# Optimization experiments

Measured on AMD Instinct MI355X. Metric: run time of the kernel, lower is better.

## Reference

```python
import jax, jax.numpy as jnp
import numpy as np

B, T, I, H, O = 64, 256, 128, 512, 64
GRAD_CLIP = 5.0


def setup_inputs() -> dict:
    key = jax.random.key(0)
    ks = jax.random.split(key, 20)
    sH = 1.0 / np.sqrt(H)
    sI = 1.0 / np.sqrt(I)
    f32 = jnp.float32
    return {
        "x": jax.random.normal(ks[0], (B, T, I), f32),
        "y": jax.random.randint(ks[1], (B,), 0, O),
        "W1w": jax.random.normal(ks[2], (H, H), f32) * sH,
        "V1w": jax.random.normal(ks[3], (H, I), f32) * sI,
        "V1b": jnp.zeros((H,), f32),
        "W2w": jax.random.normal(ks[4], (H, H), f32) * sH,
        "W2b": jnp.zeros((H,), f32),
        "V2w": jax.random.normal(ks[5], (H, I), f32) * sI,
        "W3w": jax.random.normal(ks[6], (H, H), f32) * sH,
        "W3b": jnp.zeros((H,), f32),
        "V3w": jax.random.normal(ks[7], (H, I), f32) * sI,
        "Woutw": jax.random.normal(ks[8], (O, H), f32) * sH,
        "Woutb": jnp.zeros((O,), f32),
        "BW1": jax.random.normal(ks[9], (O, H), f32) * sH,
        "BV1": jax.random.normal(ks[10], (O, H), f32) * sH,
        "BW2": jax.random.normal(ks[11], (O, H), f32) * sH,
        "BV2": jax.random.normal(ks[12], (O, H), f32) * sH,
        "BW3": jax.random.normal(ks[13], (O, H), f32) * sH,
        "BV3": jax.random.normal(ks[14], (O, H), f32) * sH,
    }


def reference(x, y, W1w, V1w, V1b, W2w, W2b, V2w, W3w, W3b, V3w,
              Woutw, Woutb, BW1, BV1, BW2, BV2, BW3, BV3):
    Bsz, Tlen, _ = x.shape
    Hd = W1w.shape[0]
    Od = Woutw.shape[0]
    h0 = jnp.zeros((Bsz, Hd), x.dtype)
    xt = jnp.swapaxes(x, 0, 1)  # [T, B, I]

    def step(h, xti):
        z = jax.nn.sigmoid(h @ W2w.T + W2b + xti @ V2w.T)
        r = jax.nn.sigmoid(h @ W3w.T + W3b + xti @ V3w.T)
        ht = jnp.tanh(xti @ V1w.T + V1b + (h * r) @ W1w.T)
        hn = (1.0 - z) * ht + z * h
        return hn, (r, z, ht, hn)

    hT, (rs, zs, hs, hid) = jax.lax.scan(step, h0, xt)  # each [T, B, H]
    output = jax.nn.softmax(hT @ Woutw.T + Woutb, axis=-1)
    error = output - jax.nn.one_hot(y, Od, dtype=output.dtype)

    BW1e, BV1e = error @ BW1, error @ BV1
    BW2e, BV2e = error @ BW2, error @ BV2
    BW3e, BV3e = error @ BW3, error @ BV3

    hiddens = jnp.concatenate([h0[None], hid], axis=0)  # [T+1, B, H]
    # Faithfully replicate torch's hiddens[t-1] list indexing: at t=0 this is
    # hiddens[-1], i.e. the FINAL hidden state (Python negative indexing).
    idx = (np.arange(Tlen) - 1) % (Tlen + 1)
    hprev = hiddens[idx]  # [T, B, H]

    rr = rs * (1.0 - rs)
    sz = 1.0 - zs
    dh = 1.0 - hs ** 2

    # z-gate terms (index 1) -- original code uses r*(1-r) here, replicated.
    zg = (hprev - hs) * rr
    zgV = zg * BV2e[None]
    zgW = zg * BW2e[None]
    dV1 = jnp.einsum('tbh,tbi->hi', zgV, xt) / Bsz
    dW1 = jnp.einsum('tbh,tbH->hH', zgW, hprev) / Bsz
    db1 = zgV.sum(0).mean(0)

    # r-gate terms (index 2)
    AV = ((BV3e[None] * sz * dh) @ W1w.T) * hprev * rr
    AW = ((BW3e[None] * sz * dh) @ W1w.T) * hprev * rr
    dV2 = jnp.einsum('tbh,tbi->hi', AV, xt) / Bsz
    dW2 = jnp.einsum('tbh,tbH->hH', AW, hprev) / Bsz
    db2 = AV.sum(0).mean(0)

    # h-gate terms (index 0)
    HV = ((BV1e[None] * sz) @ W1w.T) * dh
    HW = ((BW1e[None] * sz) @ W1w.T) * dh
    dV0 = jnp.einsum('tbh,tbi->hi', HV, xt) / Bsz
    dW0 = jnp.einsum('tbh,tbH->hH', HW, rs * hprev) / Bsz
    db0 = HV.sum(0).mean(0)

    def nc(g):
        g = g / jnp.linalg.norm(g)
        return jnp.clip(g, -GRAD_CLIP, GRAD_CLIP)

    return (output, hT,
            nc(dW0), nc(dW1), nc(dW2),
            nc(dV0), nc(dV1), nc(dV2),
            nc(db0), nc(db1), nc(db2),
            error)
```

## Files before the change

### kernel.cpp

```cpp
#include <hip/hip_runtime.h>
#include <hip/hip_bf16.h>

#define DI __device__ __forceinline__

typedef __bf16 bf16x8 __attribute__((ext_vector_type(8)));
typedef __bf16 bf16x4 __attribute__((ext_vector_type(4)));
typedef __bf16 bf16x2 __attribute__((ext_vector_type(2)));
typedef float  f32x4  __attribute__((ext_vector_type(4)));
typedef unsigned long long ull;

static constexpr int Bc = 64, Tc = 256, Ic = 128, Hc = 512, Oc = 64;
static constexpr int TBc = Tc * Bc;
static constexpr size_t THW = (size_t)TBc * Hc;

static constexpr size_t O_OUT = 0;
static constexpr size_t O_HT  = 4096;
static constexpr size_t O_DW0 = 36864;
static constexpr size_t O_DV0 = 823296;
static constexpr size_t O_DB0 = 1019904;
static constexpr size_t O_ERR = 1021440;

static constexpr size_t W_CTR  = 0;
static constexpr size_t W_SLOT = 1024;
static constexpr size_t W_DB   = 2048;
static constexpr size_t W_FLG  = 8192;
static constexpr size_t W_ERRW = 16384;
static constexpr size_t W_PROJ = 32768;
static constexpr size_t W_W1B  = 819200;
static constexpr size_t W_HX   = 1343488;
static constexpr size_t W_HRX  = 1474560;
static constexpr size_t W_XT   = 1605632;
static constexpr size_t W_HIST = 5799936;
static constexpr size_t W_PB   = 72908800;
static constexpr size_t W_NEED = W_PB + 100663296;


DI void st32_agent(float* p, float v) {
  __hip_atomic_store((unsigned int*)p, __float_as_uint(v),
                     __ATOMIC_RELAXED, __HIP_MEMORY_SCOPE_AGENT);
}
DI ull ld64_agent(const void* p) {
  return __hip_atomic_load((ull*)p, __ATOMIC_RELAXED, __HIP_MEMORY_SCOPE_AGENT);
}

DI void group_barrier(int* flags_g, int myslot, int bar, bool& dead) {
  __syncthreads();
  if (threadIdx.x == 0)
    __hip_atomic_store(&flags_g[myslot * 32], bar,
                       __ATOMIC_RELAXED, __HIP_MEMORY_SCOPE_AGENT);
  if (threadIdx.x < 64 && !dead) {
    const int l = threadIdx.x;
    int spins = 0;
    for (;;) {
      int v = bar;
      if (l < 16)
        v = __hip_atomic_load(&flags_g[l * 32],
                              __ATOMIC_RELAXED, __HIP_MEMORY_SCOPE_AGENT);
      if (__all(v >= bar)) break;
      __builtin_amdgcn_s_sleep(1);
      if (++spins > 4000000) { dead = true; break; }
    }
  }
  __syncthreads();
}

DI float hprev_at(const __bf16* __restrict__ h_h, int k, int col) {
  int t = k >> 6;
  if (t == 1) return 0.f;
  int row = (t == 0) ? (16320 + (k & 63)) : (k - 128);
  return (float)h_h[(size_t)row * 512 + col];
}


__global__ void kzero(float* __restrict__ p, int n) {
  int i = blockIdx.x * 256 + threadIdx.x;
  if (i < n) p[i] = 0.f;
}
__global__ void ksent(float* p, float v) { p[0] = v; }
__global__ void k0_cast(const float* __restrict__ s, __bf16* __restrict__ d, int n) {
  int i = blockIdx.x * 256 + threadIdx.x;
  if (i < n) d[i] = (__bf16)s[i];
}

__global__ __launch_bounds__(256)
void k1_xv(const float* __restrict__ x, const float* __restrict__ V1w,
           const float* __restrict__ V2w, const float* __restrict__ V3w,
           const float* __restrict__ V1b, const float* __restrict__ W2b,
           const float* __restrict__ W3b,
           float* __restrict__ xv1f, float* __restrict__ xv2f, float* __restrict__ xv3f)
{
  const int cb = blockIdx.x, t = blockIdx.y;
  const int g = cb >> 3, jblk = cb & 7;
  const float* Vg   = (g == 0) ? V1w : (g == 1) ? V2w : V3w;
  const float* bias = (g == 0) ? V1b : (g == 1) ? W2b : W3b;
  float* of = (g == 0) ? xv1f : (g == 1) ? xv2f : xv3f;
  __shared__ float As[64 * 69];
  __shared__ float Bs[64 * 69];
  const int tid = threadIdx.x;
  float acc[4][4] = {};
  const int m0 = (tid & 15) * 4, j0 = (tid >> 4) * 4;
  for (int kc = 0; kc < 2; ++kc) {
    __syncthreads();
    #pragma unroll
    for (int e = 0; e < 4; ++e) {
      int idx = tid + e * 256;
      int row = idx >> 4, c4 = (idx & 15) * 4;
      float4 v = *reinterpret_cast<const float4*>(&x[((size_t)row * 256 + t) * 128 + kc * 64 + c4]);
      As[row * 69 + c4 + 0] = v.x; As[row * 69 + c4 + 1] = v.y;
      As[row * 69 + c4 + 2] = v.z; As[row * 69 + c4 + 3] = v.w;
      float4 w = *reinterpret_cast<const float4*>(&Vg[(size_t)(jblk * 64 + row) * 128 + kc * 64 + c4]);
      Bs[row * 69 + c4 + 0] = w.x; Bs[row * 69 + c4 + 1] = w.y;
      Bs[row * 69 + c4 + 2] = w.z; Bs[row * 69 + c4 + 3] = w.w;
    }
    __syncthreads();
    for (int i = 0; i < 64; ++i) {
      float a[4], b[4];
      #pragma unroll
      for (int u = 0; u < 4; ++u) a[u] = As[(m0 + u) * 69 + i];
      #pragma unroll
      for (int u = 0; u < 4; ++u) b[u] = Bs[(j0 + u) * 69 + i];
      #pragma unroll
      for (int mi = 0; mi < 4; ++mi)
        #pragma unroll
        for (int ji = 0; ji < 4; ++ji) acc[mi][ji] += a[mi] * b[ji];
    }
  }
  #pragma unroll
  for (int ji = 0; ji < 4; ++ji) {
    int jg = jblk * 64 + j0 + ji;
    float bv = bias[jg];
    #pragma unroll
    for (int mi = 0; mi < 4; ++mi) {
      int b = m0 + mi;
      of[((size_t)t * 64 + b) * 512 + jg] = acc[mi][ji] + bv;
    }
  }
}

__global__ void e0_xt(const float* __restrict__ x, __bf16* __restrict__ XT)
{
  const int t = blockIdx.x;
  __shared__ __bf16 xs[64 * 132];
  const int tid = threadIdx.x;
  #pragma unroll
  for (int e = 0; e < 8; ++e) {
    int idx = tid + e * 256;
    int b = idx >> 5, c4 = (idx & 31) * 4;
    float4 v = *reinterpret_cast<const float4*>(&x[((size_t)b * 256 + t) * 128 + c4]);
    xs[b * 132 + c4 + 0] = (__bf16)v.x; xs[b * 132 + c4 + 1] = (__bf16)v.y;
    xs[b * 132 + c4 + 2] = (__bf16)v.z; xs[b * 132 + c4 + 3] = (__bf16)v.w;
  }
  __syncthreads();
  #pragma unroll
  for (int e = 0; e < 8; ++e) {
    int idx = tid + e * 256;
    int i = idx >> 4, b4 = (idx & 15) * 4;
    __bf16* d = &XT[(size_t)i * TBc + t * 64 + b4];
    d[0] = xs[(b4 + 0) * 132 + i];
    d[1] = xs[(b4 + 1) * 132 + i];
    d[2] = xs[(b4 + 2) * 132 + i];
    d[3] = xs[(b4 + 3) * 132 + i];
  }
}

__global__ __launch_bounds__(256, 1)
void k2_recur(const float* __restrict__ W1w, const float* __restrict__ W2w,
              const float* __restrict__ W3w,
              const float* __restrict__ xv1, const float* __restrict__ xv2,
              const float* __restrict__ xv3,
              __bf16* __restrict__ r_h, __bf16* __restrict__ z_h,
              __bf16* __restrict__ ht_h, __bf16* __restrict__ h_h,
              float* __restrict__ hx, float* __restrict__ hrx,
              int* __restrict__ flags, float* __restrict__ dout)
{
  const int g  = blockIdx.x >> 4;
  const int cw = blockIdx.x & 15;
  const int tid = threadIdx.x, lane = tid & 63, wv = tid >> 6;
  const int kh = wv & 1;
  const int ct = wv >> 1;
  const int q  = lane >> 4;
  const int colc = cw * 32 + ct * 16 + (lane & 15);
  const bool owner = (kh == 0);

  __shared__ __align__(16) __bf16 c0[8192];
  __shared__ __align__(16) __bf16 c1[8192];
  __shared__ __align__(16) __bf16 c2[8192];
  __shared__ float pbuf[128 * 9];

  bf16x8 w1c[3][8], w2c[3][8], w3c[3][8];
  #pragma unroll
  for (int kk2 = 0; kk2 < 8; ++kk2) {
    const int kb = (kh * 8 + kk2) * 32 + q * 8;
    #pragma unroll
    for (int j = 0; j < 8; ++j) {
      float w = W1w[(size_t)colc * 512 + kb + j];
      __bf16 a = (__bf16)w; float r1 = w - (float)a;
      __bf16 b = (__bf16)r1;
      w1c[0][kk2][j] = a; w1c[1][kk2][j] = b; w1c[2][kk2][j] = (__bf16)(r1 - (float)b);
      w = W2w[(size_t)colc * 512 + kb + j];
      a = (__bf16)w; r1 = w - (float)a; b = (__bf16)r1;
      w2c[0][kk2][j] = a; w2c[1][kk2][j] = b; w2c[2][kk2][j] = (__bf16)(r1 - (float)b);
      w = W3w[(size_t)colc * 512 + kb + j];
      a = (__bf16)w; r1 = w - (float)a; b = (__bf16)r1;
      w3c[0][kk2][j] = a; w3c[1][kk2][j] = b; w3c[2][kk2][j] = (__bf16)(r1 - (float)b);
    }
  }
  for (int i = tid; i < 8192; i += 256) {
    c0[i] = (__bf16)0.f; c1[i] = (__bf16)0.f; c2[i] = (__bf16)0.f;
  }
  __syncthreads();

  float hreg[4] = {0.f, 0.f, 0.f, 0.f};
  float* hx_g  = hx  + g * 8192;
  float* hrx_g = hrx + g * 8192;
  int* flags_g = flags + g * 16 * 32;
  const int fragbase = (colc >> 5) * 512 + (((colc >> 3) & 3) * 16 + q * 4) * 8 + (colc & 7);
  const int pb = (ct * 64 + lane) * 9;

  auto stage = [&](const float* __restrict__ srcf) {
    const ull* src = reinterpret_cast<const ull*>(srcf);
    ull u[16];
    #pragma unroll
    for (int j = 0; j < 16; ++j) u[j] = ld64_agent(src + j * 256 + tid);
    #pragma unroll
    for (int j = 0; j < 16; ++j) {
      float f0 = __uint_as_float((unsigned int)u[j]);
      float f1 = __uint_as_float((unsigned int)(u[j] >> 32));
      __bf16 a0 = (__bf16)f0; float r0 = f0 - (float)a0; __bf16 b0 = (__bf16)r0;
      __bf16 d0 = (__bf16)(r0 - (float)b0);
      __bf16 a1 = (__bf16)f1; float r1 = f1 - (float)a1; __bf16 b1 = (__bf16)r1;
      __bf16 d1 = (__bf16)(r1 - (float)b1);
      int o = (j * 256 + tid) * 2;
      bf16x2 v0; v0[0] = a0; v0[1] = a1;
      bf16x2 v1; v1[0] = b0; v1[1] = b1;
      bf16x2 v2; v2[0] = d0; v2[1] = d1;
      *reinterpret_cast<bf16x2*>(&c0[o]) = v0;
      *reinterpret_cast<bf16x2*>(&c1[o]) = v1;
      *reinterpret_cast<bf16x2*>(&c2[o]) = v2;
    }
  };

  bool dead = false;
  int bar = 0;
  #pragma unroll 1
  for (int t = 0; t < Tc; ++t) {
    const size_t rowb = ((size_t)t * 64 + g * 16 + q * 4) * 512 + colc;
    float xv1v[4], xv2v[4], xv3v[4];
    if (owner) {
      #pragma unroll
      for (int i = 0; i < 4; ++i) {
        size_t o = rowb + (size_t)i * 512;
        xv1v[i] = xv1[o]; xv2v[i] = xv2[o]; xv3v[i] = xv3[o];
      }
    }
    f32x4 a2 = {0.f,0.f,0.f,0.f}, a3 = {0.f,0.f,0.f,0.f};
    #pragma unroll
    for (int kk2 = 0; kk2 < 8; ++kk2) {
      const int idx = (kh * 8 + kk2) * 512 + lane * 8;
      bf16x8 h0 = *reinterpret_cast<const bf16x8*>(&c0[idx]);
      bf16x8 h1 = *reinterpret_cast<const bf16x8*>(&c1[idx]);
      bf16x8 h2 = *reinterpret_cast<const bf16x8*>(&c2[idx]);
      a2 = __builtin_amdgcn_mfma_f32_16x16x32_bf16(h0, w2c[0][kk2], a2, 0, 0, 0);
      a2 = __builtin_amdgcn_mfma_f32_16x16x32_bf16(h1, w2c[0][kk2], a2, 0, 0, 0);
      a2 = __builtin_amdgcn_mfma_f32_16x16x32_bf16(h0, w2c[1][kk2], a2, 0, 0, 0);
      a2 = __builtin_amdgcn_mfma_f32_16x16x32_bf16(h2, w2c[0][kk2], a2, 0, 0, 0);
      a2 = __builtin_amdgcn_mfma_f32_16x16x32_bf16(h1, w2c[1][kk2], a2, 0, 0, 0);
      a2 = __builtin_amdgcn_mfma_f32_16x16x32_bf16(h0, w2c[2][kk2], a2, 0, 0, 0);
      a3 = __builtin_amdgcn_mfma_f32_16x16x32_bf16(h0, w3c[0][kk2], a3, 0, 0, 0);
      a3 = __builtin_amdgcn_mfma_f32_16x16x32_bf16(h1, w3c[0][kk2], a3, 0, 0, 0);
      a3 = __builtin_amdgcn_mfma_f32_16x16x32_bf16(h0, w3c[1][kk2], a3, 0, 0, 0);
      a3 = __builtin_amdgcn_mfma_f32_16x16x32_bf16(h2, w3c[0][kk2], a3, 0, 0, 0);
      a3 = __builtin_amdgcn_mfma_f32_16x16x32_bf16(h1, w3c[1][kk2], a3, 0, 0, 0);
      a3 = __builtin_amdgcn_mfma_f32_16x16x32_bf16(h0, w3c[2][kk2], a3, 0, 0, 0);
    }
    if (!owner) {
      #pragma unroll
      for (int i = 0; i < 4; ++i) { pbuf[pb + i] = a2[i]; pbuf[pb + 4 + i] = a3[i]; }
    }
    __syncthreads();
    float zz[4], rr4[4];
    if (owner) {
      #pragma unroll
      for (int i = 0; i < 4; ++i) {
        float s2 = a2[i] + pbuf[pb + i]     + xv2v[i];
        float s3 = a3[i] + pbuf[pb + 4 + i] + xv3v[i];
        zz[i]  = 1.f / (1.f + expf(-s2));
        rr4[i] = 1.f / (1.f + expf(-s3));
        st32_agent(&hrx_g[fragbase + i * 8], hreg[i] * rr4[i]);
      }
      #pragma unroll
      for (int i = 0; i < 4; ++i) {
        z_h[rowb + (size_t)i * 512] = (__bf16)zz[i];
        r_h[rowb + (size_t)i * 512] = (__bf16)rr4[i];
      }
    }
    ++bar; group_barrier(flags_g, cw, bar, dead);
    stage(hrx_g);
    __syncthreads();
    f32x4 a1 = {0.f,0.f,0.f,0.f};
    #pragma unroll
    for (int kk2 = 0; kk2 < 8; ++kk2) {
      const int idx = (kh * 8 + kk2) * 512 + lane * 8;
      bf16x8 h0 = *reinterpret_cast<const bf16x8*>(&c0[idx]);
      bf16x8 h1 = *reinterpret_cast<const bf16x8*>(&c1[idx]);
      bf16x8 h2 = *reinterpret_cast<const bf16x8*>(&c2[idx]);
      a1 = __builtin_amdgcn_mfma_f32_16x16x32_bf16(h0, w1c[0][kk2], a1, 0, 0, 0);
      a1 = __builtin_amdgcn_mfma_f32_16x16x32_bf16(h1, w1c[0][kk2], a1, 0, 0, 0);
      a1 = __builtin_amdgcn_mfma_f32_16x16x32_bf16(h0, w1c[1][kk2], a1, 0, 0, 0);
      a1 = __builtin_amdgcn_mfma_f32_16x16x32_bf16(h2, w1c[0][kk2], a1, 0, 0, 0);
      a1 = __builtin_amdgcn_mfma_f32_16x16x32_bf16(h1, w1c[1][kk2], a1, 0, 0, 0);
      a1 = __builtin_amdgcn_mfma_f32_16x16x32_bf16(h0, w1c[2][kk2], a1, 0, 0, 0);
    }
    if (!owner) {
      #pragma unroll
      for (int i = 0; i < 4; ++i) pbuf[pb + i] = a1[i];
    }
    __syncthreads();
    if (owner) {
      float htv[4];
      #pragma unroll
      for (int i = 0; i < 4; ++i) {
        float pre = a1[i] + pbuf[pb + i] + xv1v[i];
        float ht = tanhf(pre);
        float hn = zz[i] * (hreg[i] - ht) + ht;
        htv[i] = ht;
        hreg[i] = hn;
        st32_agent(&hx_g[fragbase + i * 8], hn);
      }
      #pragma unroll
      for (int i = 0; i < 4; ++i) {
        ht_h[rowb + (size_t)i * 512] = (__bf16)htv[i];
        h_h[rowb + (size_t)i * 512]  = (__bf16)hreg[i];
      }
    }
    ++bar; group_barrier(flags_g, cw, bar, dead);
    stage(hx_g);
    __syncthreads();
  }
  if (owner) {
    #pragma unroll
    for (int i = 0; i < 4; ++i) {
      int b = g * 16 + q * 4 + i;
      dout[O_HT + (size_t)b * 512 + colc] = hreg[i];
    }
  }
}

__global__ void k3a_soft(const float* __restrict__ Woutw, const float* __restrict__ Woutb,
                         const int* __restrict__ y, float* __restrict__ dout,
                         float* __restrict__ errw)
{
  const int b = blockIdx.x, o = threadIdx.x;
  const float* hrow = dout + O_HT + (size_t)b * 512;
  float sv = Woutb[o];
  for (int k = 0; k < 512; ++k) sv += hrow[k] * Woutw[(size_t)o * 512 + k];
  float mx = sv;
  for (int off = 32; off; off >>= 1) mx = fmaxf(mx, __shfl_xor(mx, off, 64));
  float e = expf(sv - mx);
  float sum = e;
  for (int off = 32; off; off >>= 1) sum += __shfl_xor(sum, off, 64);
  float outp = e / sum;
  float errv = outp - ((y[b] == o) ? 1.f : 0.f);
  dout[O_OUT + b * 64 + o] = outp;
  dout[O_ERR + b * 64 + o] = errv;
  errw[b * 64 + o] = errv;
}

__global__ __launch_bounds__(256)
void k3b_proj(const float* __restrict__ err,
              const float* b0, const float* b1, const float* b2,
              const float* b3, const float* b4, const float* b5,
              float* __restrict__ proj)
{
  const int p = blockIdx.y;
  const int hb = blockIdx.x * 64;
  const float* BX = (p==0)?b0:(p==1)?b1:(p==2)?b2:(p==3)?b3:(p==4)?b4:b5;
  __shared__ float es[64 * 64];
  __shared__ float bs[64 * 65];
  for (int i = threadIdx.x; i < 4096; i += 256) es[i] = err[i];
  for (int i = threadIdx.x; i < 4096; i += 256) {
    int o = i >> 6, hh = i & 63;
    bs[o * 65 + hh] = BX[(size_t)o * 512 + hb + hh];
  }
  __syncthreads();
  for (int e = 0; e < 16; ++e) {
    int idx = threadIdx.x + e * 256;
    int b = idx >> 6, hh = idx & 63;
    float s = 0.f;
    for (int o = 0; o < 64; ++o) s += es[b * 64 + o] * bs[o * 65 + hh];
    proj[(size_t)p * 32768 + b * 512 + hb + hh] = s;
  }
}

__global__ __launch_bounds__(256)
void e1t(const __bf16* __restrict__ r_h, const __bf16* __restrict__ h_h,
         __bf16* __restrict__ HpT, __bf16* __restrict__ RsHpT)
{
  const int t = blockIdx.y, hb = blockIdx.x * 64;
  const int tid = threadIdx.x;
  __shared__ __bf16 tr[64 * 68];
  float hpv[16], rv[16];
  #pragma unroll
  for (int e = 0; e < 16; ++e) {
    int idx = tid + e * 256;
    int b = idx >> 6, hl = idx & 63;
    hpv[e] = hprev_at(h_h, t * 64 + b, hb + hl);
    rv[e]  = (float)r_h[((size_t)t * 64 + b) * 512 + hb + hl];
  }
  for (int rnd = 0; rnd < 2; ++rnd) {
    __syncthreads();
    #pragma unroll
    for (int e = 0; e < 16; ++e) {
      int idx = tid + e * 256;
      int b = idx >> 6, hl = idx & 63;
      tr[b * 68 + hl] = (__bf16)(rnd == 0 ? hpv[e] : rv[e] * hpv[e]);
    }
    __syncthreads();
    __bf16* dst = (rnd == 0) ? HpT : RsHpT;
    #pragma unroll
    for (int e = 0; e < 16; ++e) {
      int idx = tid + e * 256;
      int hl2 = idx >> 6, b2 = idx & 63;
      dst[(size_t)(hb + hl2) * TBc + t * 64 + b2] = tr[b2 * 68 + hl2];
    }
  }
}

__global__ __launch_bounds__(256)
void k4_pgemm(const __bf16* __restrict__ z_h, const __bf16* __restrict__ ht_h,
              const __bf16* __restrict__ r_h, const __bf16* __restrict__ h_h,
              const float* __restrict__ proj, const __bf16* __restrict__ W1b,
              __bf16* __restrict__ P)
{
  const int p = blockIdx.z;
  const int krow0 = blockIdx.x * 128;
  const int n0 = blockIdx.y * 128;
  const int pidx = (p == 0) ? 5 : (p == 1) ? 4 : (p == 2) ? 1 : 0;
  const float* pr = proj + (size_t)pidx * 32768;
  const int tid = threadIdx.x, lane = tid & 63, wv = tid >> 6, q = lane >> 4;
  const int wm = (wv & 1) * 64, wn = (wv >> 1) * 64;
  __shared__ __align__(16) __bf16 Al[128 * 40];
  __shared__ __align__(16) __bf16 Bl[128 * 40];
  f32x4 acc[4][4] = {};
  for (int kt = 0; kt < 16; ++kt) {
    const int h0 = kt * 32;
    __syncthreads();
    #pragma unroll
    for (int e = 0; e < 4; ++e) {
      int idx = tid + e * 256;
      int row = idx >> 3, h4 = (idx & 7) * 4;
      int kg = krow0 + row;
      bf16x4 zz = *reinterpret_cast<const bf16x4*>(&z_h[(size_t)kg * 512 + h0 + h4]);
      bf16x4 tt = *reinterpret_cast<const bf16x4*>(&ht_h[(size_t)kg * 512 + h0 + h4]);
      float4 pv = *reinterpret_cast<const float4*>(&pr[(size_t)(kg & 63) * 512 + h0 + h4]);
      float pvv[4] = {pv.x, pv.y, pv.z, pv.w};
      bf16x4 gv;
      #pragma unroll
      for (int j = 0; j < 4; ++j) {
        float sz = 1.f - (float)zz[j];
        float v = pvv[j] * sz;
        if (p < 2) { float h = (float)tt[j]; v *= (1.f - h * h); }
        gv[j] = (__bf16)v;
      }
      *reinterpret_cast<bf16x4*>(&Al[row * 40 + h4]) = gv;
      bf16x4 wv4 = *reinterpret_cast<const bf16x4*>(&W1b[(size_t)(n0 + row) * 512 + h0 + h4]);
      *reinterpret_cast<bf16x4*>(&Bl[row * 40 + h4]) = wv4;
    }
    __syncthreads();
    bf16x8 af[4], bfv[4];
    #pragma unroll
    for (int mi = 0; mi < 4; ++mi)
      af[mi] = *reinterpret_cast<const bf16x8*>(&Al[(wm + mi * 16 + (lane & 15)) * 40 + q * 8]);
    #pragma unroll
    for (int ni = 0; ni < 4; ++ni)
      bfv[ni] = *reinterpret_cast<const bf16x8*>(&Bl[(wn + ni * 16 + (lane & 15)) * 40 + q * 8]);
    #pragma unroll
    for (int mi = 0; mi < 4; ++mi)
      #pragma unroll
      for (int ni = 0; ni < 4; ++ni)
        acc[mi][ni] = __builtin_amdgcn_mfma_f32_16x16x32_bf16(af[mi], bfv[ni], acc[mi][ni], 0, 0, 0);
  }
  __bf16* Pp = P + (size_t)p * THW;
  #pragma unroll
  for (int mi = 0; mi < 4; ++mi) {
    const int kg = krow0 + wm + mi * 16 + q * 4;
    const int tt = kg >> 6;
    #pragma unroll
    for (int ni = 0; ni < 4; ++ni) {
      const int n = n0 + wn + ni * 16 + (lane & 15);
      union { __bf16 b[4]; uint2 u; } pk;
      #pragma unroll
      for (int i = 0; i < 4; ++i) {
        float mul;
        if (p < 2) {
          float r = (float)r_h[(size_t)(kg + i) * 512 + n];
          float hp = 0.f;
          if (tt != 1) {
            int kr = (tt == 0) ? (16320 + (kg & 63) + i) : (kg + i - 128);
            hp = (float)h_h[(size_t)kr * 512 + n];
          }
          mul = hp * r * (1.f - r);
        } else {
          float h = (float)ht_h[(size_t)(kg + i) * 512 + n];
          mul = 1.f - h * h;
        }
        pk.b[i] = (__bf16)(acc[mi][ni][i] * mul);
      }
      *reinterpret_cast<uint2*>(&Pp[(size_t)n * TBc + kg]) = pk.u;
    }
  }
}

__global__ __launch_bounds__(256)
void k5_grad(const __bf16* __restrict__ Ap, int amode, const __bf16* __restrict__ Bp,
             const __bf16* __restrict__ r_h, const __bf16* __restrict__ ht_h,
             const __bf16* __restrict__ h_h, const float* __restrict__ projA,
             float* __restrict__ out, int N, int klen, float scale)
{
  const int m0 = blockIdx.x * 128;
  const int n0 = blockIdx.y * 128;
  const int tid = threadIdx.x, lane = tid & 63, wv = tid >> 6, q = lane >> 4;
  const int wm = (wv & 1) * 64, wn = (wv >> 1) * 64;
  __shared__ __align__(16) __bf16 Al[128 * 72];
  __shared__ __align__(16) __bf16 Bl[128 * 72];
  f32x4 acc[4][4] = {};
  const int iters = klen >> 6;
  for (int kt = 0; kt < iters; ++kt) {
    const int kk0 = blockIdx.z * klen + kt * 64;
    __syncthreads();
    #pragma unroll
    for (int e = 0; e < 8; ++e) {
      int idx = tid + e * 256;
      int row = idx >> 4, c4 = (idx & 15) * 4;
      bf16x4 bv = *reinterpret_cast<const bf16x4*>(&Bp[(size_t)(n0 + row) * TBc + kk0 + c4]);
      *reinterpret_cast<bf16x4*>(&Bl[row * 72 + c4]) = bv;
    }
    if (amode == 0) {
      #pragma unroll
      for (int e = 0; e < 8; ++e) {
        int idx = tid + e * 256;
        int row = idx >> 4, c4 = (idx & 15) * 4;
        bf16x4 av = *reinterpret_cast<const bf16x4*>(&Ap[(size_t)(m0 + row) * TBc + kk0 + c4]);
        *reinterpret_cast<bf16x4*>(&Al[row * 72 + c4]) = av;
      }
    } else {
      #pragma unroll
      for (int e = 0; e < 8; ++e) {
        int idx = tid + e * 256;
        int kk = idx >> 5;
        int m4 = (idx & 31) * 4;
        int kg = kk0 + kk;
        int tt = kg >> 6;
        bf16x4 hs = *reinterpret_cast<const bf16x4*>(&ht_h[(size_t)kg * 512 + m0 + m4]);
        bf16x4 rv = *reinterpret_cast<const bf16x4*>(&r_h[(size_t)kg * 512 + m0 + m4]);
        float4 pv = *reinterpret_cast<const float4*>(&projA[(size_t)(kg & 63) * 512 + m0 + m4]);
        float pvv[4] = {pv.x, pv.y, pv.z, pv.w};
        float hpf[4] = {0.f, 0.f, 0.f, 0.f};
        if (tt != 1) {
          int kr = (tt == 0) ? (16320 + (kg & 63)) : (kg - 128);
          bf16x4 hp = *reinterpret_cast<const bf16x4*>(&h_h[(size_t)kr * 512 + m0 + m4]);
          #pragma unroll
          for (int j = 0; j < 4; ++j) hpf[j] = (float)hp[j];
        }
        #pragma unroll
        for (int j = 0; j < 4; ++j) {
          float r = (float)rv[j];
          float zg = (hpf[j] - (float)hs[j]) * r * (1.f - r) * pvv[j];
          Al[(m4 + j) * 72 + kk] = (__bf16)zg;
        }
      }
    }
    __syncthreads();
    #pragma unroll
    for (int ks = 0; ks < 2; ++ks) {
      bf16x8 af[4], bfv[4];
      #pragma unroll
      for (int mi = 0; mi < 4; ++mi)
        af[mi] = *reinterpret_cast<const bf16x8*>(&Al[(wm + mi * 16 + (lane & 15)) * 72 + ks * 32 + q * 8]);
      #pragma unroll
      for (int ni = 0; ni < 4; ++ni)
        bfv[ni] = *reinterpret_cast<const bf16x8*>(&Bl[(wn + ni * 16 + (lane & 15)) * 72 + ks * 32 + q * 8]);
      #pragma unroll
      for (int mi = 0; mi < 4; ++mi)
        #pragma unroll
        for (int ni = 0; ni < 4; ++ni)
          acc[mi][ni] = __builtin_amdgcn_mfma_f32_16x16x32_bf16(af[mi], bfv[ni], acc[mi][ni], 0, 0, 0);
    }
  }
  #pragma unroll
  for (int mi = 0; mi < 4; ++mi) {
    const int m = m0 + wm + mi * 16 + q * 4;
    #pragma unroll
    for (int ni = 0; ni < 4; ++ni) {
      const int n = n0 + wn + ni * 16 + (lane & 15);
      #pragma unroll
      for (int i = 0; i < 4; ++i)
        atomicAdd(&out[(size_t)(m + i) * N + n], acc[mi][ni][i] * scale);
    }
  }
}

__global__ void k_dbP(const __bf16* __restrict__ P, float* __restrict__ db)
{
  const size_t plane = (blockIdx.y == 0) ? 2 : 0;
  const int dbo = (blockIdx.y == 0) ? 0 : 1024;
  const __bf16* row = P + plane * THW + (size_t)blockIdx.x * TBc;
  float sv = 0.f;
  for (int i = threadIdx.x; i < TBc; i += 256) sv += (float)row[i];
  for (int off = 32; off; off >>= 1) sv += __shfl_xor(sv, off, 64);
  __shared__ float red[4];
  if ((threadIdx.x & 63) == 0) red[threadIdx.x >> 6] = sv;
  __syncthreads();
  if (threadIdx.x == 0)
    atomicAdd(&db[dbo + blockIdx.x], (red[0] + red[1] + red[2] + red[3]) * (1.f / 64.f));
}

__global__ void k_dbzg(const __bf16* __restrict__ r_h, const __bf16* __restrict__ ht_h,
                       const __bf16* __restrict__ h_h, const float* __restrict__ proj,
                       float* __restrict__ db)
{
  const int hb = blockIdx.x * 64;
  const int col = hb + (threadIdx.x & 63);
  const int part = threadIdx.x >> 6;
  const int kb = blockIdx.y * 1024;
  float sum = 0.f;
  for (int k = kb + part; k < kb + 1024; k += 4) {
    float hs = (float)ht_h[(size_t)k * 512 + col];
    float r  = (float)r_h[(size_t)k * 512 + col];
    float hp = hprev_at(h_h, k, col);
    float pv = proj[3 * 32768 + (size_t)(k & 63) * 512 + col];
    sum += (hp - hs) * r * (1.f - r) * pv;
  }
  __shared__ float sred[4][64];
  sred[part][threadIdx.x & 63] = sum;
  __syncthreads();
  if (threadIdx.x < 64)
    atomicAdd(&db[512 + hb + threadIdx.x],
              (sred[0][threadIdx.x] + sred[1][threadIdx.x] +
               sred[2][threadIdx.x] + sred[3][threadIdx.x]) * (1.f / 64.f));
}

__global__ void k6a_sumsq(const float* __restrict__ dout, const float* __restrict__ db,
                          float* __restrict__ slots)
{
  const int yy = blockIdx.y;
  const float* src; int count;
  if (yy < 3)      { src = dout + O_DW0 + (size_t)yy * 262144; count = 262144; }
  else if (yy < 6) { src = dout + O_DV0 + (size_t)(yy - 3) * 65536; count = 65536; }
  else             { src = db + (size_t)(yy - 6) * 512; count = 512; }
  int start = blockIdx.x * 4096;
  if (start >= count) return;
  int end = min(start + 4096, count);
  float sp = 0.f;
  for (int i = start + threadIdx.x; i < end; i += 256) { float v = src[i]; sp += v * v; }
  for (int off = 32; off; off >>= 1) sp += __shfl_xor(sp, off, 64);
  __shared__ float red[4];
  if ((threadIdx.x & 63) == 0) red[threadIdx.x >> 6] = sp;
  __syncthreads();
  if (threadIdx.x == 0) atomicAdd(&slots[yy], red[0] + red[1] + red[2] + red[3]);
}

__global__ void k6b_write(const float* __restrict__ db,
                          const float* __restrict__ slots, float* __restrict__ dout)
{
  const int yy = blockIdx.y;
  const float* src; int count; size_t oo;
  if (yy < 3)      { oo = O_DW0 + (size_t)yy * 262144; src = dout + oo; count = 262144; }
  else if (yy < 6) { oo = O_DV0 + (size_t)(yy - 3) * 65536; src = dout + oo; count = 65536; }
  else             { oo = O_DB0 + (size_t)(yy - 6) * 512; src = db + (size_t)(yy - 6) * 512; count = 512; }
  int start = blockIdx.x * 4096;
  if (start >= count) return;
  int end = min(start + 4096, count);
  float inv = 1.f / sqrtf(slots[yy]);
  for (int i = start + threadIdx.x; i < end; i += 256) {
    float v = src[i] * inv;
    dout[oo + i] = fminf(fmaxf(v, -5.f), 5.f);
  }
}

extern "C" void kernel_launch(void* const* d_in, const int* in_sizes, int n_in,
                              void* d_out, int out_size, void* d_ws, size_t ws_size,
                              hipStream_t stream)
{
  const float* x     = (const float*)d_in[0];
  const int*   y     = (const int*)d_in[1];
  const float* W1w   = (const float*)d_in[2];
  const float* V1w   = (const float*)d_in[3];
  const float* V1b   = (const float*)d_in[4];
  const float* W2w   = (const float*)d_in[5];
  const float* W2b   = (const float*)d_in[6];
  const float* V2w   = (const float*)d_in[7];
  const float* W3w   = (const float*)d_in[8];
  const float* W3b   = (const float*)d_in[9];
  const float* V3w   = (const float*)d_in[10];
  const float* Woutw = (const float*)d_in[11];
  const float* Woutb = (const float*)d_in[12];
  const float* BW1   = (const float*)d_in[13];
  const float* BV1   = (const float*)d_in[14];
  const float* BW2   = (const float*)d_in[15];
  const float* BV2   = (const float*)d_in[16];
  const float* BW3   = (const float*)d_in[17];
  const float* BV3   = (const float*)d_in[18];
  float* dout = (float*)d_out;
  char* ws = (char*)d_ws;

  if (ws_size < W_NEED) { ksent<<<1, 1, 0, stream>>>(dout, (float)ws_size); return; }

  float*  slots = (float*)(ws + W_SLOT);
  float*  dbr   = (float*)(ws + W_DB);
  int*    flg   = (int*)(ws + W_FLG);
  float*  errw  = (float*)(ws + W_ERRW);
  float*  proj  = (float*)(ws + W_PROJ);
  __bf16* W1b   = (__bf16*)(ws + W_W1B);
  float*  hx    = (float*)(ws + W_HX);
  float*  hrx   = (float*)(ws + W_HRX);
  __bf16* XT    = (__bf16*)(ws + W_XT);
  __bf16* r_h   = (__bf16*)(ws + W_HIST);
  __bf16* z_h   = (__bf16*)(ws + W_HIST + 16777216);
  __bf16* ht_h  = (__bf16*)(ws + W_HIST + 33554432);
  __bf16* h_h   = (__bf16*)(ws + W_HIST + 50331648);
  char*   PB    = ws + W_PB;

  float* xv1 = (float*)PB;
  float* xv2 = (float*)(PB + 33554432);
  float* xv3 = (float*)(PB + 67108864);
  __bf16* P     = (__bf16*)PB;
  __bf16* HpT   = (__bf16*)(PB + 67108864);
  __bf16* RsHpT = (__bf16*)(PB + 83886080);

  kzero<<<16, 256, 0, stream>>>((float*)ws, 4096);
  kzero<<<3840, 256, 0, stream>>>(dout + O_DW0, 983040);
  k0_cast<<<1024, 256, 0, stream>>>(W1w, W1b, 262144);
  k1_xv<<<dim3(24, 256), 256, 0, stream>>>(x, V1w, V2w, V3w, V1b, W2b, W3b, xv1, xv2, xv3);
  e0_xt<<<256, 256, 0, stream>>>(x, XT);
  k2_recur<<<64, 256, 0, stream>>>(W1w, W2w, W3w, xv1, xv2, xv3,
                                   r_h, z_h, ht_h, h_h, hx, hrx, flg, dout);
  k3a_soft<<<64, 64, 0, stream>>>(Woutw, Woutb, y, dout, errw);
  k3b_proj<<<dim3(8, 6), 256, 0, stream>>>(errw, BW1, BV1, BW2, BV2, BW3, BV3, proj);
  e1t<<<dim3(8, 256), 256, 0, stream>>>(r_h, h_h, HpT, RsHpT);
  k_dbzg<<<dim3(8, 16), 256, 0, stream>>>(r_h, ht_h, h_h, proj, dbr);

  k4_pgemm<<<dim3(128, 4, 4), 256, 0, stream>>>(z_h, ht_h, r_h, h_h, proj, W1b, P);
  const float sc = 1.f / 64.f;
  k5_grad<<<dim3(4, 4, 16), 256, 0, stream>>>(P + 3 * THW, 0, RsHpT, r_h, ht_h, h_h, proj,
                                              dout + O_DW0, 512, 1024, sc);
  k5_grad<<<dim3(4, 4, 16), 256, 0, stream>>>(nullptr, 1, HpT, r_h, ht_h, h_h, proj + 2 * 32768,
                                              dout + O_DW0 + 262144, 512, 1024, sc);
  k5_grad<<<dim3(4, 4, 16), 256, 0, stream>>>(P + 1 * THW, 0, HpT, r_h, ht_h, h_h, proj,
                                              dout + O_DW0 + 524288, 512, 1024, sc);
  k5_grad<<<dim3(4, 1, 16), 256, 0, stream>>>(P + 2 * THW, 0, XT, r_h, ht_h, h_h, proj,
                                              dout + O_DV0, 128, 1024, sc);
  k5_grad<<<dim3(4, 1, 16), 256, 0, stream>>>(nullptr, 1, XT, r_h, ht_h, h_h, proj + 3 * 32768,
                                              dout + O_DV0 + 65536, 128, 1024, sc);
  k5_grad<<<dim3(4, 1, 16), 256, 0, stream>>>(P + 0 * THW, 0, XT, r_h, ht_h, h_h, proj,
                                              dout + O_DV0 + 131072, 128, 1024, sc);
  k_dbP<<<dim3(512, 2), 256, 0, stream>>>(P, dbr);
  k6a_sumsq<<<dim3(64, 9), 256, 0, stream>>>(dout, dbr, slots);
  k6b_write<<<dim3(64, 9), 256, 0, stream>>>(dbr, slots, dout);
}
```

Measured before the change: 2.705 ms.

## Replace flag barrier with epoch-tagged data exchange in recurrence kernel

The recurrent kernel no longer runs a separate flag-based group barrier before staging h and h*r. Each writer packs the three bf16 split components with an epoch tag into 32-bit words, and readers poll the data itself until every tag matches the current step. This removes one round of global flag traffic and barrier latency per half-step, and the bf16 splitting moves from readers to writers. The cost is a threefold larger exchange buffer, which is zeroed beforehand, plus repeated re-reads of the whole buffer while polling. The W1 cast is also moved to run after the recurrence, reusing the exchange memory region.

```diff
diff --git a/kernel.cpp b/kernel.cpp
--- a/kernel.cpp
+++ b/kernel.cpp
@@ -20,48 +20,29 @@
 static constexpr size_t O_DB0 = 1019904;
 static constexpr size_t O_ERR = 1021440;
 
-static constexpr size_t W_CTR  = 0;
 static constexpr size_t W_SLOT = 1024;
 static constexpr size_t W_DB   = 2048;
-static constexpr size_t W_FLG  = 8192;
 static constexpr size_t W_ERRW = 16384;
 static constexpr size_t W_PROJ = 32768;
+static constexpr size_t W_EXCH = 819200;
 static constexpr size_t W_W1B  = 819200;
-static constexpr size_t W_HX   = 1343488;
-static constexpr size_t W_HRX  = 1474560;
 static constexpr size_t W_XT   = 1605632;
 static constexpr size_t W_HIST = 5799936;
 static constexpr size_t W_PB   = 72908800;
 static constexpr size_t W_NEED = W_PB + 100663296;
 
 
-DI void st32_agent(float* p, float v) {
-  __hip_atomic_store((unsigned int*)p, __float_as_uint(v),
-                     __ATOMIC_RELAXED, __HIP_MEMORY_SCOPE_AGENT);
-}
 DI ull ld64_agent(const void* p) {
   return __hip_atomic_load((ull*)p, __ATOMIC_RELAXED, __HIP_MEMORY_SCOPE_AGENT);
 }
-
-DI void group_barrier(int* flags_g, int myslot, int bar, bool& dead) {
-  __syncthreads();
-  if (threadIdx.x == 0)
-    __hip_atomic_store(&flags_g[myslot * 32], bar,
-                       __ATOMIC_RELAXED, __HIP_MEMORY_SCOPE_AGENT);
-  if (threadIdx.x < 64 && !dead) {
-    const int l = threadIdx.x;
-    int spins = 0;
-    for (;;) {
-      int v = bar;
-      if (l < 16)
-        v = __hip_atomic_load(&flags_g[l * 32],
-                              __ATOMIC_RELAXED, __HIP_MEMORY_SCOPE_AGENT);
-      if (__all(v >= bar)) break;
-      __builtin_amdgcn_s_sleep(1);
-      if (++spins > 4000000) { dead = true; break; }
-    }
-  }
-  __syncthreads();
+DI void stu32_agent(unsigned int* p, unsigned int v) {
+  __hip_atomic_store(p, v, __ATOMIC_RELAXED, __HIP_MEMORY_SCOPE_AGENT);
+}
+DI unsigned short bfbits(__bf16 x) {
+  union { __bf16 b; unsigned short u; } c; c.b = x; return c.u;
+}
+DI unsigned int pack_xw(__bf16 x, int ep) {
+  return ((unsigned int)bfbits(x) << 16) | (unsigned int)(ep & 0xffff);
 }
 
 DI float hprev_at(const __bf16* __restrict__ h_h, int k, int col) {
@@ -170,8 +151,7 @@
               const float* __restrict__ xv3,
               __bf16* __restrict__ r_h, __bf16* __restrict__ z_h,
               __bf16* __restrict__ ht_h, __bf16* __restrict__ h_h,
-              float* __restrict__ hx, float* __restrict__ hrx,
-              int* __restrict__ flags, float* __restrict__ dout)
+              unsigned int* __restrict__ exch, float* __restrict__ dout)
 {
   const int g  = blockIdx.x >> 4;
   const int cw = blockIdx.x & 15;
@@ -211,39 +191,43 @@
   __syncthreads();
 
   float hreg[4] = {0.f, 0.f, 0.f, 0.f};
-  float* hx_g  = hx  + g * 8192;
-  float* hrx_g = hrx + g * 8192;
-  int* flags_g = flags + g * 16 * 32;
+  unsigned int* hrx_g = exch + (size_t)g * 49152;
+  unsigned int* hx_g  = hrx_g + 24576;
   const int fragbase = (colc >> 5) * 512 + (((colc >> 3) & 3) * 16 + q * 4) * 8 + (colc & 7);
   const int pb = (ct * 64 + lane) * 9;
 
-  auto stage = [&](const float* __restrict__ srcf) {
-    const ull* src = reinterpret_cast<const ull*>(srcf);
-    ull u[16];
-    #pragma unroll
-    for (int j = 0; j < 16; ++j) u[j] = ld64_agent(src + j * 256 + tid);
-    #pragma unroll
-    for (int j = 0; j < 16; ++j) {
-      float f0 = __uint_as_float((unsigned int)u[j]);
-      float f1 = __uint_as_float((unsigned int)(u[j] >> 32));
-      __bf16 a0 = (__bf16)f0; float r0 = f0 - (float)a0; __bf16 b0 = (__bf16)r0;
-      __bf16 d0 = (__bf16)(r0 - (float)b0);
-      __bf16 a1 = (__bf16)f1; float r1 = f1 - (float)a1; __bf16 b1 = (__bf16)r1;
-      __bf16 d1 = (__bf16)(r1 - (float)b1);
-      int o = (j * 256 + tid) * 2;
-      bf16x2 v0; v0[0] = a0; v0[1] = a1;
-      bf16x2 v1; v1[0] = b0; v1[1] = b1;
-      bf16x2 v2; v2[0] = d0; v2[1] = d1;
-      *reinterpret_cast<bf16x2*>(&c0[o]) = v0;
-      *reinterpret_cast<bf16x2*>(&c1[o]) = v1;
-      *reinterpret_cast<bf16x2*>(&c2[o]) = v2;
+  bool dead = false;
+
+  auto stage_poll = [&](const unsigned int* __restrict__ base, int ep) {
+    int spins = 0;
+    for (;;) {
+      bool ok = true;
+      #pragma unroll
+      for (int cc = 0; cc < 3; ++cc) {
+        const ull* src = reinterpret_cast<const ull*>(base + cc * 8192);
+        __bf16* dst = (cc == 0) ? c0 : (cc == 1) ? c1 : c2;
+        ull u[16];
+        #pragma unroll
+        for (int j = 0; j < 16; ++j) u[j] = ld64_agent(src + tid + j * 256);
+        #pragma unroll
+        for (int j = 0; j < 16; ++j) {
+          ok = ok && ((int)(u[j] & 0xffffu) == ep)
+                  && ((int)((u[j] >> 32) & 0xffffu) == ep);
+          int o = tid + j * 256;
+          unsigned int w = (unsigned int)((u[j] >> 16) & 0xffffu)
+                         | ((unsigned int)(u[j] >> 48) << 16);
+          *reinterpret_cast<unsigned int*>(&dst[2 * o]) = w;
+        }
+      }
+      if (dead || __all(ok)) break;
+      __builtin_amdgcn_s_sleep(1);
+      if (++spins > 1000000) { dead = true; break; }
     }
   };
 
-  bool dead = false;
-  int bar = 0;
   #pragma unroll 1
   for (int t = 0; t < Tc; ++t) {
+    const int ep = t + 1;
     const size_t rowb = ((size_t)t * 64 + g * 16 + q * 4) * 512 + colc;
     float xv1v[4], xv2v[4], xv3v[4];
     if (owner) {
@@ -286,7 +270,13 @@
         float s3 = a3[i] + pbuf[pb + 4 + i] + xv3v[i];
         zz[i]  = 1.f / (1.f + expf(-s2));
         rr4[i] = 1.f / (1.f + expf(-s3));
-        st32_agent(&hrx_g[fragbase + i * 8], hreg[i] * rr4[i]);
+        float hv = hreg[i] * rr4[i];
+        __bf16 a = (__bf16)hv; float r1 = hv - (float)a;
+        __bf16 b = (__bf16)r1; __bf16 cres = (__bf16)(r1 - (float)b);
+        int w = fragbase + i * 8;
+        stu32_agent(&hrx_g[w],          pack_xw(a, ep));
+        stu32_agent(&hrx_g[8192 + w],   pack_xw(b, ep));
+        stu32_agent(&hrx_g[16384 + w],  pack_xw(cres, ep));
       }
       #pragma unroll
       for (int i = 0; i < 4; ++i) {
@@ -294,8 +284,7 @@
         r_h[rowb + (size_t)i * 512] = (__bf16)rr4[i];
       }
     }
-    ++bar; group_barrier(flags_g, cw, bar, dead);
-    stage(hrx_g);
+    stage_poll(hrx_g, ep);
     __syncthreads();
     f32x4 a1 = {0.f,0.f,0.f,0.f};
     #pragma unroll
@@ -325,7 +314,12 @@
         float hn = zz[i] * (hreg[i] - ht) + ht;
         htv[i] = ht;
         hreg[i] = hn;
-        st32_agent(&hx_g[fragbase + i * 8], hn);
+        __bf16 a = (__bf16)hn; float r1 = hn - (float)a;
+        __bf16 b = (__bf16)r1; __bf16 cres = (__bf16)(r1 - (float)b);
+        int w = fragbase + i * 8;
+        stu32_agent(&hx_g[w],          pack_xw(a, ep));
+        stu32_agent(&hx_g[8192 + w],   pack_xw(b, ep));
+        stu32_agent(&hx_g[16384 + w],  pack_xw(cres, ep));
       }
       #pragma unroll
       for (int i = 0; i < 4; ++i) {
@@ -333,8 +327,9 @@
         h_h[rowb + (size_t)i * 512]  = (__bf16)hreg[i];
       }
     }
-    ++bar; group_barrier(flags_g, cw, bar, dead);
-    stage(hx_g);
+    if (t + 1 < Tc) {
+      stage_poll(hx_g, ep);
+    }
     __syncthreads();
   }
   if (owner) {
@@ -708,12 +703,10 @@
 
   float*  slots = (float*)(ws + W_SLOT);
   float*  dbr   = (float*)(ws + W_DB);
-  int*    flg   = (int*)(ws + W_FLG);
   float*  errw  = (float*)(ws + W_ERRW);
   float*  proj  = (float*)(ws + W_PROJ);
+  unsigned int* exch = (unsigned int*)(ws + W_EXCH);
   __bf16* W1b   = (__bf16*)(ws + W_W1B);
-  float*  hx    = (float*)(ws + W_HX);
-  float*  hrx   = (float*)(ws + W_HRX);
   __bf16* XT    = (__bf16*)(ws + W_XT);
   __bf16* r_h   = (__bf16*)(ws + W_HIST);
   __bf16* z_h   = (__bf16*)(ws + W_HIST + 16777216);
@@ -729,12 +722,13 @@
   __bf16* RsHpT = (__bf16*)(PB + 83886080);
 
   kzero<<<16, 256, 0, stream>>>((float*)ws, 4096);
+  kzero<<<768, 256, 0, stream>>>((float*)(ws + W_EXCH), 196608);
   kzero<<<3840, 256, 0, stream>>>(dout + O_DW0, 983040);
-  k0_cast<<<1024, 256, 0, stream>>>(W1w, W1b, 262144);
   k1_xv<<<dim3(24, 256), 256, 0, stream>>>(x, V1w, V2w, V3w, V1b, W2b, W3b, xv1, xv2, xv3);
   e0_xt<<<256, 256, 0, stream>>>(x, XT);
   k2_recur<<<64, 256, 0, stream>>>(W1w, W2w, W3w, xv1, xv2, xv3,
-                                   r_h, z_h, ht_h, h_h, hx, hrx, flg, dout);
+                                   r_h, z_h, ht_h, h_h, exch, dout);
+  k0_cast<<<1024, 256, 0, stream>>>(W1w, W1b, 262144);
   k3a_soft<<<64, 64, 0, stream>>>(Woutw, Woutb, y, dout, errw);
   k3b_proj<<<dim3(8, 6), 256, 0, stream>>>(errw, BW1, BV1, BW2, BV2, BW3, BV3, proj);
   e1t<<<dim3(8, 256), 256, 0, stream>>>(r_h, h_h, HpT, RsHpT);
```

After: 7.819 ms. +189.1%, slower.

## Move history stores after group barrier and merge gradient GEMMs into one launch

Applied to the files above, without the earlier changes.

In the recurrent kernel, the bf16 history stores (z, r, ht, h) now happen after the inter-block group barrier instead of before it, so they overlap with the barrier wait rather than delaying the signal. The final-step staging of hx is also skipped. The six k5_grad launches are merged into one 960-block k5_all launch, which picks its job from the block index. This cuts launch overhead and lets the small dV GEMMs fill the GPU alongside the dW GEMMs. htv is hoisted out of the owner branch so it stays in scope for the later store.

```diff
diff --git a/kernel.cpp b/kernel.cpp
--- a/kernel.cpp
+++ b/kernel.cpp
@@ -20,7 +20,6 @@
 static constexpr size_t O_DB0 = 1019904;
 static constexpr size_t O_ERR = 1021440;
 
-static constexpr size_t W_CTR  = 0;
 static constexpr size_t W_SLOT = 1024;
 static constexpr size_t W_DB   = 2048;
 static constexpr size_t W_FLG  = 8192;
@@ -288,13 +287,15 @@
         rr4[i] = 1.f / (1.f + expf(-s3));
         st32_agent(&hrx_g[fragbase + i * 8], hreg[i] * rr4[i]);
       }
+    }
+    ++bar; group_barrier(flags_g, cw, bar, dead);
+    if (owner) {
       #pragma unroll
       for (int i = 0; i < 4; ++i) {
         z_h[rowb + (size_t)i * 512] = (__bf16)zz[i];
         r_h[rowb + (size_t)i * 512] = (__bf16)rr4[i];
       }
     }
-    ++bar; group_barrier(flags_g, cw, bar, dead);
     stage(hrx_g);
     __syncthreads();
     f32x4 a1 = {0.f,0.f,0.f,0.f};
@@ -316,8 +317,8 @@
       for (int i = 0; i < 4; ++i) pbuf[pb + i] = a1[i];
     }
     __syncthreads();
+    float htv[4];
     if (owner) {
-      float htv[4];
       #pragma unroll
       for (int i = 0; i < 4; ++i) {
         float pre = a1[i] + pbuf[pb + i] + xv1v[i];
@@ -327,14 +328,16 @@
         hreg[i] = hn;
         st32_agent(&hx_g[fragbase + i * 8], hn);
       }
+    }
+    ++bar; group_barrier(flags_g, cw, bar, dead);
+    if (owner) {
       #pragma unroll
       for (int i = 0; i < 4; ++i) {
         ht_h[rowb + (size_t)i * 512] = (__bf16)htv[i];
         h_h[rowb + (size_t)i * 512]  = (__bf16)hreg[i];
       }
     }
-    ++bar; group_barrier(flags_g, cw, bar, dead);
-    stage(hx_g);
+    if (t + 1 < Tc) stage(hx_g);
     __syncthreads();
   }
   if (owner) {
@@ -512,13 +515,35 @@
 }
 
 __global__ __launch_bounds__(256)
-void k5_grad(const __bf16* __restrict__ Ap, int amode, const __bf16* __restrict__ Bp,
-             const __bf16* __restrict__ r_h, const __bf16* __restrict__ ht_h,
-             const __bf16* __restrict__ h_h, const float* __restrict__ projA,
-             float* __restrict__ out, int N, int klen, float scale)
-{
-  const int m0 = blockIdx.x * 128;
-  const int n0 = blockIdx.y * 128;
+void k5_all(const __bf16* __restrict__ P, const __bf16* __restrict__ RsHpT,
+            const __bf16* __restrict__ HpT, const __bf16* __restrict__ XT,
+            const __bf16* __restrict__ r_h, const __bf16* __restrict__ ht_h,
+            const __bf16* __restrict__ h_h, const float* __restrict__ proj,
+            float* __restrict__ dout, float scale)
+{
+  const __bf16* Ap; int amode; const __bf16* Bp; const float* projA;
+  float* out; int N; int m0i, n0i, zi;
+  int b = blockIdx.x;
+  if (b < 768) {
+    int job = b >> 8, wb = b & 255;
+    m0i = wb & 3; n0i = (wb >> 2) & 3; zi = wb >> 4;
+    N = 512;
+    out = dout + O_DW0 + (size_t)job * 262144;
+    if (job == 0)      { Ap = P + 3 * THW; amode = 0; Bp = RsHpT; projA = proj; }
+    else if (job == 1) { Ap = nullptr;     amode = 1; Bp = HpT;   projA = proj + 2 * 32768; }
+    else               { Ap = P + 1 * THW; amode = 0; Bp = HpT;   projA = proj; }
+  } else {
+    int b2 = b - 768; int job = b2 >> 6, wb = b2 & 63;
+    m0i = wb & 3; n0i = 0; zi = wb >> 2;
+    N = 128;
+    out = dout + O_DV0 + (size_t)job * 65536;
+    if (job == 0)      { Ap = P + 2 * THW; amode = 0; Bp = XT; projA = proj; }
+    else if (job == 1) { Ap = nullptr;     amode = 1; Bp = XT; projA = proj + 3 * 32768; }
+    else               { Ap = P + 0 * THW; amode = 0; Bp = XT; projA = proj; }
+  }
+  const int m0 = m0i * 128;
+  const int n0 = n0i * 128;
+  const int klen = 1024;
   const int tid = threadIdx.x, lane = tid & 63, wv = tid >> 6, q = lane >> 4;
   const int wm = (wv & 1) * 64, wn = (wv >> 1) * 64;
   __shared__ __align__(16) __bf16 Al[128 * 72];
@@ -526,7 +551,7 @@
   f32x4 acc[4][4] = {};
   const int iters = klen >> 6;
   for (int kt = 0; kt < iters; ++kt) {
-    const int kk0 = blockIdx.z * klen + kt * 64;
+    const int kk0 = zi * klen + kt * 64;
     __syncthreads();
     #pragma unroll
     for (int e = 0; e < 8; ++e) {
@@ -742,18 +767,7 @@
 
   k4_pgemm<<<dim3(128, 4, 4), 256, 0, stream>>>(z_h, ht_h, r_h, h_h, proj, W1b, P);
   const float sc = 1.f / 64.f;
-  k5_grad<<<dim3(4, 4, 16), 256, 0, stream>>>(P + 3 * THW, 0, RsHpT, r_h, ht_h, h_h, proj,
-                                              dout + O_DW0, 512, 1024, sc);
-  k5_grad<<<dim3(4, 4, 16), 256, 0, stream>>>(nullptr, 1, HpT, r_h, ht_h, h_h, proj + 2 * 32768,
-                                              dout + O_DW0 + 262144, 512, 1024, sc);
-  k5_grad<<<dim3(4, 4, 16), 256, 0, stream>>>(P + 1 * THW, 0, HpT, r_h, ht_h, h_h, proj,
-                                              dout + O_DW0 + 524288, 512, 1024, sc);
-  k5_grad<<<dim3(4, 1, 16), 256, 0, stream>>>(P + 2 * THW, 0, XT, r_h, ht_h, h_h, proj,
-                                              dout + O_DV0, 128, 1024, sc);
-  k5_grad<<<dim3(4, 1, 16), 256, 0, stream>>>(nullptr, 1, XT, r_h, ht_h, h_h, proj + 3 * 32768,
-                                              dout + O_DV0 + 65536, 128, 1024, sc);
-  k5_grad<<<dim3(4, 1, 16), 256, 0, stream>>>(P + 0 * THW, 0, XT, r_h, ht_h, h_h, proj,
-                                              dout + O_DV0 + 131072, 128, 1024, sc);
+  k5_all<<<960, 256, 0, stream>>>(P, RsHpT, HpT, XT, r_h, ht_h, h_h, proj, dout, sc);
   k_dbP<<<dim3(512, 2), 256, 0, stream>>>(P, dbr);
   k6a_sumsq<<<dim3(64, 9), 256, 0, stream>>>(dout, dbr, slots);
   k6b_write<<<dim3(64, 9), 256, 0, stream>>>(dbr, slots, dout);
```

Result: faster. 2.583 ms (-4.5%).
